# Kernel tuning notes

Measured on AMD Instinct MI355X. Metric: run time of the kernel, lower is better.

Reference implementation:

```python
import jax, jax.numpy as jnp
import numpy as np


def mha_col0(x0, w_in, b_in, w_out, b_out):
    # x0: [N, D]. torch MHA (1 head, batch_first=False): seq dim = N, this is the
    # batch-0 slice (the only one consumed by tmp[:, 0]).
    qkv = x0 @ w_in.T + b_in                     # [N, 3D]
    q, k, v = jnp.split(qkv, 3, axis=-1)         # each [N, D]
    scale = 1.0 / np.sqrt(np.float32(q.shape[-1]))
    attn = jax.nn.softmax((q * scale) @ k.T, axis=-1)   # [N, N]
    return (attn @ v) @ w_out.T + b_out          # [N, D]


def sage(x_src, x_dst, ei, w_l, b_l, w_r):
    # PyG SAGEConv with aggr='sum': out = lin_l(sum_j x_src[src_j]) + lin_r(x_dst)
    msg = x_src[ei[0]]                                            # [E, D] gather
    agg = jax.ops.segment_sum(msg, ei[1], num_segments=x_dst.shape[0])  # [Nd, D] scatter
    return agg @ w_l.T + b_l + x_dst @ w_r.T


def setup_inputs() -> dict:
    key = jax.random.key(0)
    ks = jax.random.split(key, 24)
    N, C, D, E = 8192, 6, 128, 262144
    s = 0.05
    p = lambda k, shape: jax.random.normal(k, shape, dtype=jnp.float32) * s
    return {
        "x_A": jax.random.normal(ks[0], (N, C, D), dtype=jnp.float32),
        "x_B": jax.random.normal(ks[1], (N, C, D), dtype=jnp.float32),
        "ei_AB": jax.random.randint(ks[2], (2, E), 0, N),
        "ei_BA": jax.random.randint(ks[3], (2, E), 0, N),
        "ei_AA": jax.random.randint(ks[4], (2, E), 0, N),
        "inW_A": p(ks[5], (3 * D, D)), "inB_A": p(ks[6], (3 * D,)),
        "outW_A": p(ks[7], (D, D)), "outB_A": p(ks[8], (D,)),
        "inW_B": p(ks[9], (3 * D, D)), "inB_B": p(ks[10], (3 * D,)),
        "outW_B": p(ks[11], (D, D)), "outB_B": p(ks[12], (D,)),
        "wl_AB": p(ks[13], (D, D)), "bl_AB": p(ks[14], (D,)), "wr_AB": p(ks[15], (D, D)),
        "wl_BA": p(ks[16], (D, D)), "bl_BA": p(ks[17], (D,)), "wr_BA": p(ks[18], (D, D)),
        "wl_AA": p(ks[19], (D, D)), "bl_AA": p(ks[20], (D,)), "wr_AA": p(ks[21], (D, D)),
    }


def reference(x_A, x_B, ei_AB, ei_BA, ei_AA,
              inW_A, inB_A, outW_A, outB_A,
              inW_B, inB_B, outW_B, outB_B,
              wl_AB, bl_AB, wr_AB,
              wl_BA, bl_BA, wr_BA,
              wl_AA, bl_AA, wr_AA):
    # per-type attention, keeping only column 0 (tmp[:, 0])
    h_A = mha_col0(x_A[:, 0], inW_A, inB_A, outW_A, outB_A)   # [N, D]
    h_B = mha_col0(x_B[:, 0], inW_B, inB_B, outW_B, outB_B)   # [N, D]
    # HeteroConv(aggr='sum'): B gets A->B; A gets B->A + A->A
    out_B = sage(h_A, h_B, ei_AB, wl_AB, bl_AB, wr_AB)
    out_A = (sage(h_B, h_A, ei_BA, wl_BA, bl_BA, wr_BA)
             + sage(h_A, h_A, ei_AA, wl_AA, bl_AA, wr_AA))
    # re-attach remaining column tokens (x is 3D)
    new_A = jnp.concatenate((out_A[:, None, :], x_A[:, 1:]), axis=1)  # [N, C, D]
    new_B = jnp.concatenate((out_B[:, None, :], x_B[:, 1:]), axis=1)
    return new_A, new_B
```

## Files before the change

### kernel.cpp

```cpp
#include <hip/hip_runtime.h>
#include <hip/hip_bf16.h>

typedef unsigned short u16;
typedef unsigned int u32;
typedef __attribute__((ext_vector_type(8))) short bf16x8;
typedef __attribute__((ext_vector_type(4))) short bf16x4;
typedef __attribute__((ext_vector_type(4))) float f32x4;
typedef __attribute__((ext_vector_type(16))) float f32x16;

#define MFMA(a,b,c)   __builtin_amdgcn_mfma_f32_16x16x32_bf16((a),(b),(c),0,0,0)
#define MFMA32(a,b,c) __builtin_amdgcn_mfma_f32_32x32x16_bf16((a),(b),(c),0,0,0)

__device__ __forceinline__ float bf2f(u16 u){
  union { float f; u32 i; } c; c.i = ((u32)u) << 16; return c.f;
}
__device__ __forceinline__ u16 f2bf(float f){
  __hip_bfloat16 h = __float2bfloat16(f);
  u16 u; __builtin_memcpy(&u, &h, 2); return u;
}
__device__ __forceinline__ bf16x8 ld8f(const float* p){
  bf16x8 r;
  #pragma unroll
  for (int i = 0; i < 8; i++) r[i] = (short)f2bf(p[i]);
  return r;
}
__device__ __forceinline__ u32 cvtpk(float a, float b){
  u32 r; asm volatile("v_cvt_pk_bf16_f32 %0, %1, %2" : "=v"(r) : "v"(a), "v"(b)); return r;
}
__device__ __forceinline__ void pl32swap(u32 &a, u32 &b){
  asm volatile("v_permlane32_swap_b32 %0, %1" : "+v"(a), "+v"(b));
}

struct WPrepArgs { const float* src[10]; int off[10]; int total4; };
__global__ __launch_bounds__(256) void prelude_kernel(
    WPrepArgs a, u16* __restrict__ wdst,
    const int* __restrict__ e0, const int* __restrict__ e1, const int* __restrict__ e2,
    int* __restrict__ cnt,
    const float* __restrict__ xA, float* __restrict__ outA,
    const float* __restrict__ xB, float* __restrict__ outB,
    int Nn, int E, int W, int HB, int TB)
{
  const int tid = threadIdx.x;
  int b = blockIdx.x;
  if (b < W) {
    int i = b * 256 + tid;
    if (i >= a.total4) return;
    int e = i * 4;
    int j = 0;
    #pragma unroll
    for (int k = 1; k < 10; k++) if (e >= a.off[k]) j = k;
    f32x4 v = *(const f32x4*)(a.src[j] + (e - a.off[j]));
    bf16x4 o;
    #pragma unroll
    for (int r = 0; r < 4; r++) o[r] = (short)f2bf(v[r]);
    *(bf16x4*)(wdst + e) = o;
    return;
  }
  b -= W;
  if (b < 3 * HB) {
    int t = b / HB;
    int e = (b % HB) * 256 + tid;
    if (e >= E) return;
    const int* ei = t == 0 ? e0 : (t == 1 ? e1 : e2);
    atomicAdd(&cnt[t * Nn + ei[E + e]], 1);
    return;
  }
  b -= 3 * HB;
  {
    int t = b / TB;
    int idx = (b % TB) * 256 + tid;
    if (idx >= Nn * 160) return;
    const float* x = t ? xB : xA;
    float* o = t ? outB : outA;
    int n = idx / 160, r = idx % 160;
    size_t off = (size_t)n * 768 + 128 + (size_t)r * 4;
    *(f32x4*)(o + off) = *(const f32x4*)(x + off);
  }
}

template<int XBF>
__global__ __launch_bounds__(256) void linear_kernel(
    const void* __restrict__ xA_, const u16* __restrict__ wA, const float* __restrict__ bA, u16* __restrict__ yA,
    const void* __restrict__ xB_, const u16* __restrict__ wB, const float* __restrict__ bB, u16* __restrict__ yB,
    u16* __restrict__ vtA_, u16* __restrict__ vtB_,
    int xstride, int ystride, int M, int N)
{
  const void* x_ = blockIdx.y ? xB_ : xA_;
  const u16* w = blockIdx.y ? wB : wA;
  const float* b = blockIdx.y ? bB : bA;
  u16* y = blockIdx.y ? yB : yA;
  u16* vt = blockIdx.y ? vtB_ : vtA_;
  const int lane = threadIdx.x & 63, wid = threadIdx.x >> 6;
  const int g = lane >> 4, l15 = lane & 15;
  const int row0 = blockIdx.x * 64 + wid * 16;

  bf16x8 a[4];
  if (XBF) {
    const u16* xr = (const u16*)x_ + (size_t)(row0 + l15) * xstride;
    #pragma unroll
    for (int kk = 0; kk < 4; kk++) a[kk] = *(const bf16x8*)(xr + kk * 32 + g * 8);
  } else {
    const float* xr = (const float*)x_ + (size_t)(row0 + l15) * xstride;
    #pragma unroll
    for (int kk = 0; kk < 4; kk++) a[kk] = ld8f(xr + kk * 32 + g * 8);
  }

  const f32x4 fz = {0.f, 0.f, 0.f, 0.f};
  for (int j0 = 0; j0 < M; j0 += 16) {
    f32x4 acc = fz;
    const u16* wr_ = w + (size_t)(j0 + l15) * 128;
    #pragma unroll
    for (int kk = 0; kk < 4; kk++)
      acc = MFMA(a[kk], *(const bf16x8*)(wr_ + kk * 32 + g * 8), acc);
    float bv = b[j0 + l15];
    if (j0 < 256 || vt == nullptr) {
      #pragma unroll
      for (int r = 0; r < 4; r++)
        y[(size_t)(row0 + g * 4 + r) * ystride + j0 + l15] = f2bf(acc[r] + bv);
    } else {
      bf16x4 o4;
      #pragma unroll
      for (int r = 0; r < 4; r++) o4[r] = (short)f2bf(acc[r] + bv);
      *(bf16x4*)(vt + (size_t)(j0 - 256 + l15) * N + row0 + g * 4) = o4;
    }
  }
}

__global__ __launch_bounds__(256, 2) void flash_kernel(
    const u16* __restrict__ qkvA, const u16* __restrict__ vtA,
    const u16* __restrict__ qkvB, const u16* __restrict__ vtB,
    u16* __restrict__ part_acc, float* __restrict__ part_ml,
    int N, int segsz, int SEG)
{
  __shared__ __align__(16) u16 Kt[2][64 * 128];
  __shared__ __align__(16) u16 Vtt[2][128 * 64];
  const int ty = blockIdx.z;
  const u16* qkv = ty ? qkvB : qkvA;
  const u16* vt  = ty ? vtB  : vtA;
  const int tid = threadIdx.x;
  const int lane = tid & 63, wid = tid >> 6;
  const int l31 = lane & 31, h = lane >> 5, l7 = lane & 7;
  const int q = blockIdx.x * 128 + wid * 32 + l31;
  const int seg = blockIdx.y;
  const int kvbase = seg * segsz;
  const float C = 0.088388347648318447f * 1.4426950408889634f;
  const float THR = 8.0f / C;

  int rk[4], ck[4], cks[4], rv[4], cv[4], cvs[4];
  #pragma unroll
  for (int i = 0; i < 4; i++) {
    int ch = tid + i * 256;
    rk[i] = ch >> 4; ck[i] = (ch & 15) * 8; cks[i] = ck[i] ^ ((rk[i] & 7) << 3);
    rv[i] = ch >> 3; cv[i] = (ch & 7) * 8;  cvs[i] = cv[i] ^ ((rv[i] & 7) << 3);
  }

  bf16x8 aQ[8];
  const u16* qr = qkv + (size_t)q * 256;
  #pragma unroll
  for (int kk = 0; kk < 8; kk++) aQ[kk] = *(const bf16x8*)(qr + kk * 16 + h * 8);

  f32x16 accO[4];
  #pragma unroll
  for (int d = 0; d < 4; d++) accO[d] = (f32x16)0.f;
  float m_ = -INFINITY, l_ = 0.f;

  {
    #pragma unroll
    for (int i = 0; i < 4; i++) {
      bf16x8 kv8 = *(const bf16x8*)(qkv + 128 + (size_t)(kvbase + rk[i]) * 256 + ck[i]);
      bf16x8 vv8 = *(const bf16x8*)(vt + (size_t)rv[i] * N + kvbase + cv[i]);
      *(bf16x8*)&Kt[0][rk[i] * 128 + cks[i]] = kv8;
      *(bf16x8*)&Vtt[0][rv[i] * 64 + cvs[i]] = vv8;
    }
  }
  __syncthreads();

  int cur = 0;
  for (int kt = 0; kt < segsz; kt += 64) {
    const bool pfch = (kt + 64 < segsz);
    bf16x8 kreg[4], vreg[4];
    if (pfch) {
      const int kv0n = kvbase + kt + 64;
      #pragma unroll
      for (int i = 0; i < 4; i++) {
        kreg[i] = *(const bf16x8*)(qkv + 128 + (size_t)(kv0n + rk[i]) * 256 + ck[i]);
        vreg[i] = *(const bf16x8*)(vt + (size_t)rv[i] * N + kv0n + cv[i]);
      }
    }

    const u16* KtC = Kt[cur];
    const u16* VtC = Vtt[cur];

    f32x16 sc0 = (f32x16)0.f, sc1 = (f32x16)0.f;
    __builtin_amdgcn_s_setprio(1);
    #pragma unroll
    for (int kk = 0; kk < 8; kk++) {
      const int co = ((kk * 2 + h) * 8) ^ (l7 << 3);
      bf16x8 aK0 = *(bf16x8*)&KtC[l31 * 128 + co];
      bf16x8 aK1 = *(bf16x8*)&KtC[(32 + l31) * 128 + co];
      sc0 = MFMA32(aK0, aQ[kk], sc0);
      sc1 = MFMA32(aK1, aQ[kk], sc1);
    }
    __builtin_amdgcn_s_setprio(0);

    float pmax = sc0[0];
    #pragma unroll
    for (int i = 1; i < 16; i++) pmax = fmaxf(pmax, sc0[i]);
    #pragma unroll
    for (int i = 0; i < 16; i++) pmax = fmaxf(pmax, sc1[i]);
    pmax = fmaxf(pmax, __shfl_xor(pmax, 32));
    if (!__all(pmax - m_ <= THR)) {
      float nm = fmaxf(m_, pmax);
      float corr = __builtin_exp2f((m_ - nm) * C);
      m_ = nm; l_ *= corr;
      #pragma unroll
      for (int d = 0; d < 4; d++)
        #pragma unroll
        for (int i = 0; i < 16; i++) accO[d][i] *= corr;
    }
    float sum = 0.f;
    #pragma unroll
    for (int i = 0; i < 16; i++) {
      float e0 = __builtin_exp2f((sc0[i] - m_) * C);
      float e1 = __builtin_exp2f((sc1[i] - m_) * C);
      sc0[i] = e0; sc1[i] = e1; sum += e0 + e1;
    }
    sum += __shfl_xor(sum, 32);
    l_ += sum;

    #pragma unroll
    for (int t = 0; t < 4; t++) {
      const int jA = (t & 1) * 2, jB = jA + 1;
      u32 a0, b0, a1, b1;
      if (t < 2) {
        a0 = cvtpk(sc0[jA * 4 + 0], sc0[jA * 4 + 1]);
        b0 = cvtpk(sc0[jB * 4 + 0], sc0[jB * 4 + 1]);
        a1 = cvtpk(sc0[jA * 4 + 2], sc0[jA * 4 + 3]);
        b1 = cvtpk(sc0[jB * 4 + 2], sc0[jB * 4 + 3]);
      } else {
        a0 = cvtpk(sc1[jA * 4 + 0], sc1[jA * 4 + 1]);
        b0 = cvtpk(sc1[jB * 4 + 0], sc1[jB * 4 + 1]);
        a1 = cvtpk(sc1[jA * 4 + 2], sc1[jA * 4 + 3]);
        b1 = cvtpk(sc1[jB * 4 + 2], sc1[jB * 4 + 3]);
      }
      pl32swap(a0, b0); pl32swap(a1, b1);
      union { u32 w[4]; bf16x8 v; } pf;
      pf.w[0] = a0; pf.w[1] = a1; pf.w[2] = b0; pf.w[3] = b1;
      __builtin_amdgcn_s_setprio(1);
      #pragma unroll
      for (int db = 0; db < 4; db++) {
        bf16x8 aV = *(bf16x8*)&VtC[(db * 32 + l31) * 64 + (((t * 2 + h) * 8) ^ (l7 << 3))];
        accO[db] = MFMA32(aV, pf.v, accO[db]);
      }
      __builtin_amdgcn_s_setprio(0);
    }

    if (pfch) {
      const int nb = cur ^ 1;
      #pragma unroll
      for (int i = 0; i < 4; i++) {
        *(bf16x8*)&Kt[nb][rk[i] * 128 + cks[i]] = kreg[i];
        *(bf16x8*)&Vtt[nb][rv[i] * 64 + cvs[i]] = vreg[i];
      }
    }
    __syncthreads();
    cur ^= 1;
  }

  const size_t pbase = ((size_t)(ty * SEG + seg) * N + q) * 128;
  #pragma unroll
  for (int d = 0; d < 4; d++)
    #pragma unroll
    for (int j = 0; j < 4; j++) {
      bf16x4 o4;
      #pragma unroll
      for (int r = 0; r < 4; r++) o4[r] = (short)f2bf(accO[d][j * 4 + r]);
      *(bf16x4*)(part_acc + pbase + d * 32 + j * 8 + h * 4) = o4;
    }
  if (h == 0) {
    float2 ml; ml.x = m_; ml.y = l_;
    *(float2*)(part_ml + ((size_t)(ty * SEG + seg) * N + q) * 2) = ml;
  }
}

__global__ __launch_bounds__(256) void combine_hproj_kernel(
    const u16* __restrict__ part_acc, const float* __restrict__ part_ml,
    const u16* __restrict__ woutA, const float* __restrict__ boutA, u16* __restrict__ hA,
    const u16* __restrict__ woutB, const float* __restrict__ boutB, u16* __restrict__ hB,
    int N, int SEG)
{
  __shared__ __align__(16) u16 ot[64 * 136];
  const int t = blockIdx.y;
  const u16* w = t ? woutB : woutA;
  const float* bb = t ? boutB : boutA;
  u16* hOut = t ? hB : hA;
  const int tid = threadIdx.x;
  const int row = tid >> 2, qt = tid & 3;
  const int grow = blockIdx.x * 64 + row;
  const float C = 0.088388347648318447f * 1.4426950408889634f;

  float m = -INFINITY;
  for (int s = 0; s < SEG; s++)
    m = fmaxf(m, part_ml[((size_t)(t * SEG + s) * N + grow) * 2]);
  float l = 0.f;
  float acc[32];
  #pragma unroll
  for (int i = 0; i < 32; i++) acc[i] = 0.f;
  for (int s = 0; s < SEG; s++) {
    const float* ml = part_ml + ((size_t)(t * SEG + s) * N + grow) * 2;
    float w8 = __builtin_exp2f((ml[0] - m) * C);
    l += w8 * ml[1];
    const u16* pa = part_acc + ((size_t)(t * SEG + s) * N + grow) * 128 + qt * 32;
    #pragma unroll
    for (int j = 0; j < 4; j++) {
      bf16x8 vch = *(const bf16x8*)(pa + j * 8);
      #pragma unroll
      for (int i = 0; i < 8; i++) acc[j * 8 + i] += w8 * bf2f((u16)vch[i]);
    }
  }
  const float inv = 1.f / l;
  #pragma unroll
  for (int j = 0; j < 4; j++) {
    bf16x8 oc;
    #pragma unroll
    for (int i = 0; i < 8; i++) oc[i] = (short)f2bf(acc[j * 8 + i] * inv);
    *(bf16x8*)&ot[row * 136 + qt * 32 + j * 8] = oc;
  }
  __syncthreads();

  const int lane = tid & 63, wid = tid >> 6;
  const int g = lane >> 4, l15 = lane & 15;
  const int row0 = wid * 16;
  bf16x8 a[4];
  #pragma unroll
  for (int kk = 0; kk < 4; kk++) a[kk] = *(bf16x8*)&ot[(row0 + l15) * 136 + kk * 32 + g * 8];
  const f32x4 fz = {0.f, 0.f, 0.f, 0.f};
  for (int j0 = 0; j0 < 128; j0 += 16) {
    f32x4 acc2 = fz;
    const u16* wr_ = w + (size_t)(j0 + l15) * 128;
    #pragma unroll
    for (int kk = 0; kk < 4; kk++)
      acc2 = MFMA(a[kk], *(const bf16x8*)(wr_ + kk * 32 + g * 8), acc2);
    float bv = bb[j0 + l15];
    #pragma unroll
    for (int r = 0; r < 4; r++)
      hOut[(size_t)(blockIdx.x * 64 + row0 + g * 4 + r) * 128 + j0 + l15] = f2bf(acc2[r] + bv);
  }
}

__global__ __launch_bounds__(1024) void scan_kernel(
    const int* __restrict__ cnt, int* __restrict__ off, int* __restrict__ work, int Nn)
{
  const int t = blockIdx.x;
  const int* c = cnt + t * Nn;
  int* o = off + t * (Nn + 1);
  int* w = work + t * Nn;
  __shared__ int part[1024];
  const int tid = threadIdx.x;
  const int base = tid * 8;
  int loc[8], s = 0;
  #pragma unroll
  for (int i = 0; i < 8; i++) { loc[i] = s; s += c[base + i]; }
  part[tid] = s;
  __syncthreads();
  #pragma unroll
  for (int st = 1; st < 1024; st <<= 1) {
    int v = (tid >= st) ? part[tid - st] : 0;
    __syncthreads();
    part[tid] += v;
    __syncthreads();
  }
  int pre = (tid == 0) ? 0 : part[tid - 1];
  #pragma unroll
  for (int i = 0; i < 8; i++) { int p = pre + loc[i]; o[base + i] = p; w[base + i] = p; }
  if (tid == 1023) o[Nn] = part[1023];
}

__global__ __launch_bounds__(256) void sortedges_kernel(
    const int* __restrict__ e0, const int* __restrict__ e1, const int* __restrict__ e2,
    int* __restrict__ work, int* __restrict__ ssrc, int Nn, int E)
{
  const int t = blockIdx.y;
  const int* ei = t == 0 ? e0 : (t == 1 ? e1 : e2);
  int e = blockIdx.x * 256 + threadIdx.x;
  if (e >= E) return;
  int s = ei[e], d = ei[E + e];
  int pos = atomicAdd(&work[t * Nn + d], 1);
  ssrc[(size_t)t * E + pos] = s;
}

__global__ __launch_bounds__(256) void aggregate_kernel(
    const u16* __restrict__ h0, const u16* __restrict__ h1, const u16* __restrict__ h2,
    const int* __restrict__ off, const int* __restrict__ ssrc,
    u16* __restrict__ agg, int Nn, int E)
{
  const int t = blockIdx.y;
  const u16* h = t == 0 ? h0 : (t == 1 ? h1 : h2);
  const int* o = off + t * (Nn + 1);
  const int* ss = ssrc + (size_t)t * E;
  u16* a = agg + (size_t)t * Nn * 128;
  const int wid = threadIdx.x >> 6, lane = threadIdx.x & 63;
  const int d = blockIdx.x * 4 + wid;
  const int s0 = o[d], s1 = o[d + 1];
  float a0 = 0.f, a1 = 0.f;
  int e = s0;
  for (; e + 3 < s1; e += 4) {
    int r0 = ss[e], r1 = ss[e + 1], r2 = ss[e + 2], r3 = ss[e + 3];
    u32 v0 = *(const u32*)(h + (size_t)r0 * 128 + lane * 2);
    u32 v1 = *(const u32*)(h + (size_t)r1 * 128 + lane * 2);
    u32 v2 = *(const u32*)(h + (size_t)r2 * 128 + lane * 2);
    u32 v3 = *(const u32*)(h + (size_t)r3 * 128 + lane * 2);
    a0 += bf2f((u16)(v0 & 0xffff)) + bf2f((u16)(v1 & 0xffff)) + bf2f((u16)(v2 & 0xffff)) + bf2f((u16)(v3 & 0xffff));
    a1 += bf2f((u16)(v0 >> 16)) + bf2f((u16)(v1 >> 16)) + bf2f((u16)(v2 >> 16)) + bf2f((u16)(v3 >> 16));
  }
  for (; e < s1; e++) {
    u32 v = *(const u32*)(h + (size_t)ss[e] * 128 + lane * 2);
    a0 += bf2f((u16)(v & 0xffff));
    a1 += bf2f((u16)(v >> 16));
  }
  *(u32*)(a + (size_t)d * 128 + lane * 2) = cvtpk(a0, a1);
}

__global__ __launch_bounds__(256) void sage_out_kernel(
    const u16* __restrict__ agg1, const u16* __restrict__ wl1, const float* __restrict__ bl1,
    const u16* __restrict__ h1, const u16* __restrict__ wr1,
    const u16* __restrict__ agg2, const u16* __restrict__ wl2, const float* __restrict__ bl2,
    const u16* __restrict__ h2, const u16* __restrict__ wr2,
    float* __restrict__ out)
{
  const int lane = threadIdx.x & 63, wid = threadIdx.x >> 6;
  const int g = lane >> 4, l15 = lane & 15;
  const int row0 = blockIdx.x * 64 + wid * 16;
  const bool two = (agg2 != nullptr);

  bf16x8 a1[4], aH1[4], a2[4], aH2[4];
  const u16* ar1 = agg1 + (size_t)(row0 + l15) * 128;
  const u16* hr1 = h1 + (size_t)(row0 + l15) * 128;
  #pragma unroll
  for (int kk = 0; kk < 4; kk++) {
    a1[kk] = *(const bf16x8*)(ar1 + kk * 32 + g * 8);
    aH1[kk] = *(const bf16x8*)(hr1 + kk * 32 + g * 8);
  }
  if (two) {
    const u16* ar2 = agg2 + (size_t)(row0 + l15) * 128;
    const u16* hr2 = h2 + (size_t)(row0 + l15) * 128;
    #pragma unroll
    for (int kk = 0; kk < 4; kk++) {
      a2[kk] = *(const bf16x8*)(ar2 + kk * 32 + g * 8);
      aH2[kk] = *(const bf16x8*)(hr2 + kk * 32 + g * 8);
    }
  }

  const f32x4 fz = {0.f, 0.f, 0.f, 0.f};
  for (int j0 = 0; j0 < 128; j0 += 16) {
    f32x4 acc = fz;
    const u16* w1 = wl1 + (size_t)(j0 + l15) * 128;
    const u16* w2 = wr1 + (size_t)(j0 + l15) * 128;
    #pragma unroll
    for (int kk = 0; kk < 4; kk++) {
      acc = MFMA(a1[kk], *(const bf16x8*)(w1 + kk * 32 + g * 8), acc);
      acc = MFMA(aH1[kk], *(const bf16x8*)(w2 + kk * 32 + g * 8), acc);
    }
    float bias = bl1[j0 + l15];
    if (two) {
      const u16* w3 = wl2 + (size_t)(j0 + l15) * 128;
      const u16* w4 = wr2 + (size_t)(j0 + l15) * 128;
      #pragma unroll
      for (int kk = 0; kk < 4; kk++) {
        acc = MFMA(a2[kk], *(const bf16x8*)(w3 + kk * 32 + g * 8), acc);
        acc = MFMA(aH2[kk], *(const bf16x8*)(w4 + kk * 32 + g * 8), acc);
      }
      bias += bl2[j0 + l15];
    }
    #pragma unroll
    for (int r = 0; r < 4; r++)
      out[(size_t)(row0 + g * 4 + r) * 768 + j0 + l15] = acc[r] + bias;
  }
}

extern "C" void kernel_launch(void* const* d_in, const int* in_sizes, int n_in,
                              void* d_out, int out_size, void* d_ws, size_t ws_size,
                              hipStream_t stream)
{
  const int D = 128, C = 6;
  const int N = in_sizes[0] / (C * D);
  const int E = in_sizes[2] / 2;

  const float* xA = (const float*)d_in[0];
  const float* xB = (const float*)d_in[1];
  const int* eiAB = (const int*)d_in[2];
  const int* eiBA = (const int*)d_in[3];
  const int* eiAA = (const int*)d_in[4];
  const float* inW_A  = (const float*)d_in[5];
  const float* inB_A  = (const float*)d_in[6];
  const float* outW_A = (const float*)d_in[7];
  const float* outB_A = (const float*)d_in[8];
  const float* inW_B  = (const float*)d_in[9];
  const float* inB_B  = (const float*)d_in[10];
  const float* outW_B = (const float*)d_in[11];
  const float* outB_B = (const float*)d_in[12];
  const float* wlAB = (const float*)d_in[13];
  const float* blAB = (const float*)d_in[14];
  const float* wrAB = (const float*)d_in[15];
  const float* wlBA = (const float*)d_in[16];
  const float* blBA = (const float*)d_in[17];
  const float* wrBA = (const float*)d_in[18];
  const float* wlAA = (const float*)d_in[19];
  const float* blAA = (const float*)d_in[20];
  const float* wrAA = (const float*)d_in[21];

  u16* qkvA = (u16*)d_ws;
  u16* qkvB = qkvA + (size_t)N * 256;
  u16* vtA  = qkvB + (size_t)N * 256;
  u16* vtB  = vtA + (size_t)D * N;
  u16* hA   = vtB + (size_t)D * N;
  u16* hB   = hA + (size_t)N * D;
  u16* wbf  = hB + (size_t)N * D;
  const int wsz[10] = {3*D*D, 3*D*D, D*D, D*D, D*D, D*D, D*D, D*D, D*D, D*D};
  const float* wsrc[10] = {inW_A, inW_B, outW_A, outW_B, wlAB, wrAB, wlBA, wrBA, wlAA, wrAA};
  WPrepArgs wp; int wtot = 0;
  for (int k = 0; k < 10; k++) { wp.src[k] = wsrc[k]; wp.off[k] = wtot; wtot += wsz[k]; }
  wp.total4 = wtot / 4;
  u16* w_inA  = wbf + wp.off[0];
  u16* w_inB  = wbf + wp.off[1];
  u16* w_outA = wbf + wp.off[2];
  u16* w_outB = wbf + wp.off[3];
  u16* w_wlAB = wbf + wp.off[4];
  u16* w_wrAB = wbf + wp.off[5];
  u16* w_wlBA = wbf + wp.off[6];
  u16* w_wrBA = wbf + wp.off[7];
  u16* w_wlAA = wbf + wp.off[8];
  u16* w_wrAA = wbf + wp.off[9];

  int* cnt  = (int*)(wbf + wtot);
  int* off  = cnt + 3 * N;
  int* work = off + 3 * (N + 1);
  int* ssrc = work + 3 * N;
  char* uni = (char*)(ssrc + 3 * E);
  size_t base_b = (size_t)(uni - (char*)d_ws);
  size_t agg_b = (size_t)3 * N * 128 * 2;
  auto part_b = [&](int S){ return (size_t)2 * S * N * 128 * 2 + (size_t)2 * S * N * 2 * 4; };
  int SEG = 4;
  while (SEG > 1 && ws_size < base_b + (part_b(SEG) > agg_b ? part_b(SEG) : agg_b)) SEG >>= 1;
  const int segsz = N / SEG;
  u16* part_acc = (u16*)uni;
  float* part_ml = (float*)(part_acc + (size_t)2 * SEG * N * 128);
  u16* aggAB = (u16*)uni;
  u16* aggBA = aggAB + (size_t)N * D;
  u16* aggAA = aggBA + (size_t)N * D;

  float* outA = (float*)d_out;
  float* outB = outA + (size_t)N * C * D;

  dim3 blk(256);
  const int W = (wp.total4 + 255) / 256;
  const int HB = (E + 255) / 256;
  const int TB = (N * 160 + 255) / 256;
  (void)hipMemsetAsync(cnt, 0, (size_t)3 * N * sizeof(int), stream);
  prelude_kernel<<<dim3(W + 3 * HB + 2 * TB), blk, 0, stream>>>(
      wp, wbf, eiAB, eiBA, eiAA, cnt, xA, outA, xB, outB, N, E, W, HB, TB);
  scan_kernel<<<dim3(3), dim3(1024), 0, stream>>>(cnt, off, work, N);
  sortedges_kernel<<<dim3(HB, 3), blk, 0, stream>>>(eiAB, eiBA, eiAA, work, ssrc, N, E);
  linear_kernel<0><<<dim3(N / 64, 2), blk, 0, stream>>>(xA, w_inA, inB_A, qkvA,
                                                        xB, w_inB, inB_B, qkvB,
                                                        vtA, vtB, C * D, 256, 384, N);
  flash_kernel<<<dim3(N / 128, SEG, 2), blk, 0, stream>>>(qkvA, vtA, qkvB, vtB,
                                                          part_acc, part_ml, N, segsz, SEG);
  combine_hproj_kernel<<<dim3(N / 64, 2), blk, 0, stream>>>(part_acc, part_ml,
                                                            w_outA, outB_A, hA,
                                                            w_outB, outB_B, hB, N, SEG);
  aggregate_kernel<<<dim3(N / 4, 3), blk, 0, stream>>>(hA, hB, hA, off, ssrc, aggAB, N, E);
  sage_out_kernel<<<dim3(N / 64), blk, 0, stream>>>(aggAB, w_wlAB, blAB, hB, w_wrAB,
                                                    nullptr, nullptr, nullptr, nullptr, nullptr, outB);
  sage_out_kernel<<<dim3(N / 64), blk, 0, stream>>>(aggBA, w_wlBA, blBA, hA, w_wrBA,
                                                    aggAA, w_wlAA, blAA, hA, w_wrAA, outA);
}
```

Baseline: 270.3 us.

## Fuse scan/sort into QKV and flash kernels, software-pipeline flash QK^T, prescale Q

Several changes land together. The edge-count scan now runs as extra blocks in the QKV projection kernel, and the edge sort runs as extra blocks in the flash attention kernel, which removes two launches. The two SAGE output launches become one 2-D launch. Q is prescaled by softmax_scale*log2(e) in the projection, so the flash and combine kernels drop the per-element multiply. The flash loop is restructured so the next tile's QK^T MFMAs are issued before the current tile's softmax and PV, using a triple-buffered V tile and ping-pong score registers. This adds register and LDS pressure. It also makes correctness rely on the scan finishing before the sort blocks run, which now holds only through stream ordering.

Measured after the change: 236.1 us. 12.6% less time.

```diff
diff --git a/kernel.cpp b/kernel.cpp
--- a/kernel.cpp
+++ b/kernel.cpp
@@ -30,6 +30,8 @@
 __device__ __forceinline__ void pl32swap(u32 &a, u32 &b){
   asm volatile("v_permlane32_swap_b32 %0, %1" : "+v"(a), "+v"(b));
 }
+
+#define QSCALE 0.12751741528681559f
 
 struct WPrepArgs { const float* src[10]; int off[10]; int total4; };
 __global__ __launch_bounds__(256) void prelude_kernel(
@@ -78,45 +80,71 @@
   }
 }
 
-template<int XBF>
-__global__ __launch_bounds__(256) void linear_kernel(
-    const void* __restrict__ xA_, const u16* __restrict__ wA, const float* __restrict__ bA, u16* __restrict__ yA,
-    const void* __restrict__ xB_, const u16* __restrict__ wB, const float* __restrict__ bB, u16* __restrict__ yB,
+__global__ __launch_bounds__(256) void qkv_scan_kernel(
+    const float* __restrict__ xA, const u16* __restrict__ wA, const float* __restrict__ bA, u16* __restrict__ yA,
+    const float* __restrict__ xB, const u16* __restrict__ wB, const float* __restrict__ bB, u16* __restrict__ yB,
     u16* __restrict__ vtA_, u16* __restrict__ vtB_,
-    int xstride, int ystride, int M, int N)
-{
-  const void* x_ = blockIdx.y ? xB_ : xA_;
-  const u16* w = blockIdx.y ? wB : wA;
-  const float* b = blockIdx.y ? bB : bA;
-  u16* y = blockIdx.y ? yB : yA;
-  u16* vt = blockIdx.y ? vtB_ : vtA_;
-  const int lane = threadIdx.x & 63, wid = threadIdx.x >> 6;
+    const int* __restrict__ cnt, int* __restrict__ off, int* __restrict__ work,
+    int Nn, int N, int LB)
+{
+  const int tid = threadIdx.x;
+  int b = blockIdx.x;
+  if (b >= 2 * LB) {
+    const int t = b - 2 * LB;
+    const int* c = cnt + t * Nn;
+    int* o = off + t * (Nn + 1);
+    int* w = work + t * Nn;
+    __shared__ int part[256];
+    const int base = tid * 32;
+    int loc[32], s = 0;
+    #pragma unroll
+    for (int i = 0; i < 32; i++) { loc[i] = s; s += c[base + i]; }
+    part[tid] = s;
+    __syncthreads();
+    #pragma unroll
+    for (int st = 1; st < 256; st <<= 1) {
+      int v = (tid >= st) ? part[tid - st] : 0;
+      __syncthreads();
+      part[tid] += v;
+      __syncthreads();
+    }
+    int pre = (tid == 0) ? 0 : part[tid - 1];
+    #pragma unroll
+    for (int i = 0; i < 32; i++) { int p = pre + loc[i]; o[base + i] = p; w[base + i] = p; }
+    if (tid == 255) o[Nn] = part[255];
+    return;
+  }
+  const int yb = b & 1, xb = b >> 1;
+  const float* x = yb ? xB : xA;
+  const u16* w = yb ? wB : wA;
+  const float* bb = yb ? bB : bA;
+  u16* y = yb ? yB : yA;
+  u16* vt = yb ? vtB_ : vtA_;
+  const int lane = tid & 63, wid = tid >> 6;
   const int g = lane >> 4, l15 = lane & 15;
-  const int row0 = blockIdx.x * 64 + wid * 16;
+  const int row0 = xb * 64 + wid * 16;
 
   bf16x8 a[4];
-  if (XBF) {
-    const u16* xr = (const u16*)x_ + (size_t)(row0 + l15) * xstride;
-    #pragma unroll
-    for (int kk = 0; kk < 4; kk++) a[kk] = *(const bf16x8*)(xr + kk * 32 + g * 8);
-  } else {
-    const float* xr = (const float*)x_ + (size_t)(row0 + l15) * xstride;
-    #pragma unroll
-    for (int kk = 0; kk < 4; kk++) a[kk] = ld8f(xr + kk * 32 + g * 8);
-  }
+  const float* xr = x + (size_t)(row0 + l15) * 768;
+  #pragma unroll
+  for (int kk = 0; kk < 4; kk++) a[kk] = ld8f(xr + kk * 32 + g * 8);
 
   const f32x4 fz = {0.f, 0.f, 0.f, 0.f};
-  for (int j0 = 0; j0 < M; j0 += 16) {
+  for (int j0 = 0; j0 < 384; j0 += 16) {
     f32x4 acc = fz;
     const u16* wr_ = w + (size_t)(j0 + l15) * 128;
     #pragma unroll
     for (int kk = 0; kk < 4; kk++)
       acc = MFMA(a[kk], *(const bf16x8*)(wr_ + kk * 32 + g * 8), acc);
-    float bv = b[j0 + l15];
-    if (j0 < 256 || vt == nullptr) {
+    float bv = bb[j0 + l15];
+    if (j0 < 128) {
       #pragma unroll
       for (int r = 0; r < 4; r++)
-        y[(size_t)(row0 + g * 4 + r) * ystride + j0 + l15] = f2bf(acc[r] + bv);
+        y[(size_t)(row0 + g * 4 + r) * 256 + j0 + l15] = f2bf((acc[r] + bv) * QSCALE);
+    } else if (j0 < 256) {
+      #pragma unroll
+      for (int r = 0; r < 4; r++)
+        y[(size_t)(row0 + g * 4 + r) * 256 + j0 + l15] = f2bf(acc[r] + bv);
     } else {
       bf16x4 o4;
       #pragma unroll
@@ -126,25 +154,40 @@
   }
 }
 
-__global__ __launch_bounds__(256, 2) void flash_kernel(
+__global__ __launch_bounds__(256, 2) void flash_sort_kernel(
     const u16* __restrict__ qkvA, const u16* __restrict__ vtA,
     const u16* __restrict__ qkvB, const u16* __restrict__ vtB,
     u16* __restrict__ part_acc, float* __restrict__ part_ml,
-    int N, int segsz, int SEG)
+    const int* __restrict__ e0, const int* __restrict__ e1, const int* __restrict__ e2,
+    int* __restrict__ work, int* __restrict__ ssrc,
+    int N, int segsz, int SEG, int NB128, int FB, int HB, int E)
 {
   __shared__ __align__(16) u16 Kt[2][64 * 128];
-  __shared__ __align__(16) u16 Vtt[2][128 * 64];
-  const int ty = blockIdx.z;
+  __shared__ __align__(16) u16 Vtt[3][128 * 64];
+  const int tid = threadIdx.x;
+  int b = blockIdx.x;
+  if (b >= FB) {
+    int sb = b - FB;
+    int t = sb / HB;
+    int e = (sb % HB) * 256 + tid;
+    if (e >= E) return;
+    const int* ei = t == 0 ? e0 : (t == 1 ? e1 : e2);
+    int s = ei[e], d = ei[E + e];
+    int pos = atomicAdd(&work[t * N + d], 1);
+    ssrc[(size_t)t * E + pos] = s;
+    return;
+  }
+  const int x = b % NB128;
+  const int rest = b / NB128;
+  const int seg = rest % SEG;
+  const int ty = rest / SEG;
   const u16* qkv = ty ? qkvB : qkvA;
   const u16* vt  = ty ? vtB  : vtA;
-  const int tid = threadIdx.x;
   const int lane = tid & 63, wid = tid >> 6;
   const int l31 = lane & 31, h = lane >> 5, l7 = lane & 7;
-  const int q = blockIdx.x * 128 + wid * 32 + l31;
-  const int seg = blockIdx.y;
+  const int q = x * 128 + wid * 32 + l31;
   const int kvbase = seg * segsz;
-  const float C = 0.088388347648318447f * 1.4426950408889634f;
-  const float THR = 8.0f / C;
+  const int nt = segsz >> 6;
 
   int rk[4], ck[4], cks[4], rv[4], cv[4], cvs[4];
   #pragma unroll
@@ -163,55 +206,79 @@
   #pragma unroll
   for (int d = 0; d < 4; d++) accO[d] = (f32x16)0.f;
   float m_ = -INFINITY, l_ = 0.f;
-
-  {
+  f32x16 scA[2], scB[2];
+  bf16x8 kreg[4], vreg[4];
+
+  #pragma unroll
+  for (int i = 0; i < 4; i++) {
+    kreg[i] = *(const bf16x8*)(qkv + 128 + (size_t)(kvbase + rk[i]) * 256 + ck[i]);
+    vreg[i] = *(const bf16x8*)(vt + (size_t)rv[i] * N + kvbase + cv[i]);
+  }
+  #pragma unroll
+  for (int i = 0; i < 4; i++) {
+    *(bf16x8*)&Kt[0][rk[i] * 128 + cks[i]] = kreg[i];
+    *(bf16x8*)&Vtt[0][rv[i] * 64 + cvs[i]] = vreg[i];
+  }
+  __syncthreads();
+  if (nt > 1) {
+    const int kv1 = kvbase + 64;
     #pragma unroll
     for (int i = 0; i < 4; i++) {
-      bf16x8 kv8 = *(const bf16x8*)(qkv + 128 + (size_t)(kvbase + rk[i]) * 256 + ck[i]);
-      bf16x8 vv8 = *(const bf16x8*)(vt + (size_t)rv[i] * N + kvbase + cv[i]);
-      *(bf16x8*)&Kt[0][rk[i] * 128 + cks[i]] = kv8;
-      *(bf16x8*)&Vtt[0][rv[i] * 64 + cvs[i]] = vv8;
-    }
-  }
-  __syncthreads();
-
-  int cur = 0;
-  for (int kt = 0; kt < segsz; kt += 64) {
-    const bool pfch = (kt + 64 < segsz);
-    bf16x8 kreg[4], vreg[4];
-    if (pfch) {
-      const int kv0n = kvbase + kt + 64;
+      kreg[i] = *(const bf16x8*)(qkv + 128 + (size_t)(kv1 + rk[i]) * 256 + ck[i]);
+      vreg[i] = *(const bf16x8*)(vt + (size_t)rv[i] * N + kv1 + cv[i]);
+    }
+  }
+  scA[0] = (f32x16)0.f; scA[1] = (f32x16)0.f;
+  #pragma unroll
+  for (int kk = 0; kk < 8; kk++) {
+    const int co = ((kk * 2 + h) * 8) ^ (l7 << 3);
+    bf16x8 aK0 = *(bf16x8*)&Kt[0][l31 * 128 + co];
+    bf16x8 aK1 = *(bf16x8*)&Kt[0][(32 + l31) * 128 + co];
+    scA[0] = MFMA32(aK0, aQ[kk], scA[0]);
+    scA[1] = MFMA32(aK1, aQ[kk], scA[1]);
+  }
+
+  int t = 0, vb = 0;
+  auto fstep = [&](f32x16* scIn, f32x16* scOut) {
+    const bool hasN = (t + 1 < nt);
+    const int kbN = (t + 1) & 1;
+    const int vbN = (vb + 1 == 3) ? 0 : vb + 1;
+    if (hasN) {
+      #pragma unroll
+      for (int i = 0; i < 4; i++) {
+        *(bf16x8*)&Kt[kbN][rk[i] * 128 + cks[i]] = kreg[i];
+        *(bf16x8*)&Vtt[vbN][rv[i] * 64 + cvs[i]] = vreg[i];
+      }
+    }
+    __syncthreads();
+    if (t + 2 < nt) {
+      const int kv0n = kvbase + (t + 2) * 64;
       #pragma unroll
       for (int i = 0; i < 4; i++) {
         kreg[i] = *(const bf16x8*)(qkv + 128 + (size_t)(kv0n + rk[i]) * 256 + ck[i]);
         vreg[i] = *(const bf16x8*)(vt + (size_t)rv[i] * N + kv0n + cv[i]);
       }
     }
-
-    const u16* KtC = Kt[cur];
-    const u16* VtC = Vtt[cur];
-
-    f32x16 sc0 = (f32x16)0.f, sc1 = (f32x16)0.f;
-    __builtin_amdgcn_s_setprio(1);
-    #pragma unroll
-    for (int kk = 0; kk < 8; kk++) {
-      const int co = ((kk * 2 + h) * 8) ^ (l7 << 3);
-      bf16x8 aK0 = *(bf16x8*)&KtC[l31 * 128 + co];
-      bf16x8 aK1 = *(bf16x8*)&KtC[(32 + l31) * 128 + co];
-      sc0 = MFMA32(aK0, aQ[kk], sc0);
-      sc1 = MFMA32(aK1, aQ[kk], sc1);
-    }
-    __builtin_amdgcn_s_setprio(0);
-
-    float pmax = sc0[0];
-    #pragma unroll
-    for (int i = 1; i < 16; i++) pmax = fmaxf(pmax, sc0[i]);
-    #pragma unroll
-    for (int i = 0; i < 16; i++) pmax = fmaxf(pmax, sc1[i]);
+    if (hasN) {
+      scOut[0] = (f32x16)0.f; scOut[1] = (f32x16)0.f;
+      #pragma unroll
+      for (int kk = 0; kk < 8; kk++) {
+        const int co = ((kk * 2 + h) * 8) ^ (l7 << 3);
+        bf16x8 aK0 = *(bf16x8*)&Kt[kbN][l31 * 128 + co];
+        bf16x8 aK1 = *(bf16x8*)&Kt[kbN][(32 + l31) * 128 + co];
+        scOut[0] = MFMA32(aK0, aQ[kk], scOut[0]);
+        scOut[1] = MFMA32(aK1, aQ[kk], scOut[1]);
+      }
+    }
+    float pmax = scIn[0][0];
+    #pragma unroll
+    for (int i = 1; i < 16; i++) pmax = fmaxf(pmax, scIn[0][i]);
+    #pragma unroll
+    for (int i = 0; i < 16; i++) pmax = fmaxf(pmax, scIn[1][i]);
     pmax = fmaxf(pmax, __shfl_xor(pmax, 32));
-    if (!__all(pmax - m_ <= THR)) {
+    if (!__all(pmax - m_ <= 8.0f)) {
       float nm = fmaxf(m_, pmax);
-      float corr = __builtin_exp2f((m_ - nm) * C);
+      float corr = __builtin_exp2f(m_ - nm);
       m_ = nm; l_ *= corr;
       #pragma unroll
       for (int d = 0; d < 4; d++)
@@ -221,51 +288,32 @@
     float sum = 0.f;
     #pragma unroll
     for (int i = 0; i < 16; i++) {
-      float e0 = __builtin_exp2f((sc0[i] - m_) * C);
-      float e1 = __builtin_exp2f((sc1[i] - m_) * C);
-      sc0[i] = e0; sc1[i] = e1; sum += e0 + e1;
+      float e0 = __builtin_exp2f(scIn[0][i] - m_);
+      float e1 = __builtin_exp2f(scIn[1][i] - m_);
+      scIn[0][i] = e0; scIn[1][i] = e1; sum += e0 + e1;
     }
     sum += __shfl_xor(sum, 32);
     l_ += sum;
-
-    #pragma unroll
-    for (int t = 0; t < 4; t++) {
-      const int jA = (t & 1) * 2, jB = jA + 1;
-      u32 a0, b0, a1, b1;
-      if (t < 2) {
-        a0 = cvtpk(sc0[jA * 4 + 0], sc0[jA * 4 + 1]);
-        b0 = cvtpk(sc0[jB * 4 + 0], sc0[jB * 4 + 1]);
-        a1 = cvtpk(sc0[jA * 4 + 2], sc0[jA * 4 + 3]);
-        b1 = cvtpk(sc0[jB * 4 + 2], sc0[jB * 4 + 3]);
-      } else {
-        a0 = cvtpk(sc1[jA * 4 + 0], sc1[jA * 4 + 1]);
-        b0 = cvtpk(sc1[jB * 4 + 0], sc1[jB * 4 + 1]);
-        a1 = cvtpk(sc1[jA * 4 + 2], sc1[jA * 4 + 3]);
-        b1 = cvtpk(sc1[jB * 4 + 2], sc1[jB * 4 + 3]);
-      }
+    #pragma unroll
+    for (int tt = 0; tt < 4; tt++) {
+      const f32x16& s_ = scIn[tt >> 1];
+      const int jA = (tt & 1) * 2, jB = jA + 1;
+      u32 a0 = cvtpk(s_[jA * 4 + 0], s_[jA * 4 + 1]);
+      u32 b0 = cvtpk(s_[jB * 4 + 0], s_[jB * 4 + 1]);
+      u32 a1 = cvtpk(s_[jA * 4 + 2], s_[jA * 4 + 3]);
+      u32 b1 = cvtpk(s_[jB * 4 + 2], s_[jB * 4 + 3]);
       pl32swap(a0, b0); pl32swap(a1, b1);
       union { u32 w[4]; bf16x8 v; } pf;
       pf.w[0] = a0; pf.w[1] = a1; pf.w[2] = b0; pf.w[3] = b1;
-      __builtin_amdgcn_s_setprio(1);
       #pragma unroll
       for (int db = 0; db < 4; db++) {
-        bf16x8 aV = *(bf16x8*)&VtC[(db * 32 + l31) * 64 + (((t * 2 + h) * 8) ^ (l7 << 3))];
+        bf16x8 aV = *(bf16x8*)&Vtt[vb][(db * 32 + l31) * 64 + (((tt * 2 + h) * 8) ^ (l7 << 3))];
         accO[db] = MFMA32(aV, pf.v, accO[db]);
       }
-      __builtin_amdgcn_s_setprio(0);
-    }
-
-    if (pfch) {
-      const int nb = cur ^ 1;
-      #pragma unroll
-      for (int i = 0; i < 4; i++) {
-        *(bf16x8*)&Kt[nb][rk[i] * 128 + cks[i]] = kreg[i];
-        *(bf16x8*)&Vtt[nb][rv[i] * 64 + cvs[i]] = vreg[i];
-      }
-    }
-    __syncthreads();
-    cur ^= 1;
-  }
+    }
+    vb = vbN; ++t;
+  };
+  while (t < nt) { fstep(scA, scB); fstep(scB, scA); }
 
   const size_t pbase = ((size_t)(ty * SEG + seg) * N + q) * 128;
   #pragma unroll
@@ -297,7 +345,6 @@
   const int tid = threadIdx.x;
   const int row = tid >> 2, qt = tid & 3;
   const int grow = blockIdx.x * 64 + row;
-  const float C = 0.088388347648318447f * 1.4426950408889634f;
 
   float m = -INFINITY;
   for (int s = 0; s < SEG; s++)
@@ -308,7 +355,7 @@
   for (int i = 0; i < 32; i++) acc[i] = 0.f;
   for (int s = 0; s < SEG; s++) {
     const float* ml = part_ml + ((size_t)(t * SEG + s) * N + grow) * 2;
-    float w8 = __builtin_exp2f((ml[0] - m) * C);
+    float w8 = __builtin_exp2f(ml[0] - m);
     l += w8 * ml[1];
     const u16* pa = part_acc + ((size_t)(t * SEG + s) * N + grow) * 128 + qt * 32;
     #pragma unroll
@@ -346,47 +393,6 @@
     for (int r = 0; r < 4; r++)
       hOut[(size_t)(blockIdx.x * 64 + row0 + g * 4 + r) * 128 + j0 + l15] = f2bf(acc2[r] + bv);
   }
-}
-
-__global__ __launch_bounds__(1024) void scan_kernel(
-    const int* __restrict__ cnt, int* __restrict__ off, int* __restrict__ work, int Nn)
-{
-  const int t = blockIdx.x;
-  const int* c = cnt + t * Nn;
-  int* o = off + t * (Nn + 1);
-  int* w = work + t * Nn;
-  __shared__ int part[1024];
-  const int tid = threadIdx.x;
-  const int base = tid * 8;
-  int loc[8], s = 0;
-  #pragma unroll
-  for (int i = 0; i < 8; i++) { loc[i] = s; s += c[base + i]; }
-  part[tid] = s;
-  __syncthreads();
-  #pragma unroll
-  for (int st = 1; st < 1024; st <<= 1) {
-    int v = (tid >= st) ? part[tid - st] : 0;
-    __syncthreads();
-    part[tid] += v;
-    __syncthreads();
-  }
-  int pre = (tid == 0) ? 0 : part[tid - 1];
-  #pragma unroll
-  for (int i = 0; i < 8; i++) { int p = pre + loc[i]; o[base + i] = p; w[base + i] = p; }
-  if (tid == 1023) o[Nn] = part[1023];
-}
-
-__global__ __launch_bounds__(256) void sortedges_kernel(
-    const int* __restrict__ e0, const int* __restrict__ e1, const int* __restrict__ e2,
-    int* __restrict__ work, int* __restrict__ ssrc, int Nn, int E)
-{
-  const int t = blockIdx.y;
-  const int* ei = t == 0 ? e0 : (t == 1 ? e1 : e2);
-  int e = blockIdx.x * 256 + threadIdx.x;
-  if (e >= E) return;
-  int s = ei[e], d = ei[E + e];
-  int pos = atomicAdd(&work[t * Nn + d], 1);
-  ssrc[(size_t)t * E + pos] = s;
 }
 
 __global__ __launch_bounds__(256) void aggregate_kernel(
@@ -422,18 +428,27 @@
 }
 
 __global__ __launch_bounds__(256) void sage_out_kernel(
-    const u16* __restrict__ agg1, const u16* __restrict__ wl1, const float* __restrict__ bl1,
-    const u16* __restrict__ h1, const u16* __restrict__ wr1,
-    const u16* __restrict__ agg2, const u16* __restrict__ wl2, const float* __restrict__ bl2,
-    const u16* __restrict__ h2, const u16* __restrict__ wr2,
-    float* __restrict__ out)
-{
+    const u16* __restrict__ aggAB, const u16* __restrict__ wlAB, const float* __restrict__ blAB,
+    const u16* __restrict__ hB, const u16* __restrict__ wrAB,
+    const u16* __restrict__ aggBA, const u16* __restrict__ wlBA, const float* __restrict__ blBA,
+    const u16* __restrict__ hA, const u16* __restrict__ wrBA,
+    const u16* __restrict__ aggAA, const u16* __restrict__ wlAA, const float* __restrict__ blAA,
+    const u16* __restrict__ wrAA,
+    float* __restrict__ outA, float* __restrict__ outB)
+{
+  const bool two = (blockIdx.y == 1);
+  const u16* agg1 = two ? aggBA : aggAB;
+  const u16* wl1  = two ? wlBA  : wlAB;
+  const float* bl1 = two ? blBA : blAB;
+  const u16* h1   = two ? hA : hB;
+  const u16* wr1  = two ? wrBA : wrAB;
+  float* out = two ? outA : outB;
+
   const int lane = threadIdx.x & 63, wid = threadIdx.x >> 6;
   const int g = lane >> 4, l15 = lane & 15;
   const int row0 = blockIdx.x * 64 + wid * 16;
-  const bool two = (agg2 != nullptr);
-
-  bf16x8 a1[4], aH1[4], a2[4], aH2[4];
+
+  bf16x8 a1[4], aH1[4], a2[4];
   const u16* ar1 = agg1 + (size_t)(row0 + l15) * 128;
   const u16* hr1 = h1 + (size_t)(row0 + l15) * 128;
   #pragma unroll
@@ -442,13 +457,10 @@
     aH1[kk] = *(const bf16x8*)(hr1 + kk * 32 + g * 8);
   }
   if (two) {
-    const u16* ar2 = agg2 + (size_t)(row0 + l15) * 128;
-    const u16* hr2 = h2 + (size_t)(row0 + l15) * 128;
-    #pragma unroll
-    for (int kk = 0; kk < 4; kk++) {
+    const u16* ar2 = aggAA + (size_t)(row0 + l15) * 128;
+    #pragma unroll
+    for (int kk = 0; kk < 4; kk++)
       a2[kk] = *(const bf16x8*)(ar2 + kk * 32 + g * 8);
-      aH2[kk] = *(const bf16x8*)(hr2 + kk * 32 + g * 8);
-    }
   }
 
   const f32x4 fz = {0.f, 0.f, 0.f, 0.f};
@@ -463,14 +475,14 @@
     }
     float bias = bl1[j0 + l15];
     if (two) {
-      const u16* w3 = wl2 + (size_t)(j0 + l15) * 128;
-      const u16* w4 = wr2 + (size_t)(j0 + l15) * 128;
+      const u16* w3 = wlAA + (size_t)(j0 + l15) * 128;
+      const u16* w4 = wrAA + (size_t)(j0 + l15) * 128;
       #pragma unroll
       for (int kk = 0; kk < 4; kk++) {
         acc = MFMA(a2[kk], *(const bf16x8*)(w3 + kk * 32 + g * 8), acc);
-        acc = MFMA(aH2[kk], *(const bf16x8*)(w4 + kk * 32 + g * 8), acc);
+        acc = MFMA(aH1[kk], *(const bf16x8*)(w4 + kk * 32 + g * 8), acc);
       }
-      bias += bl2[j0 + l15];
+      bias += blAA[j0 + l15];
     }
     #pragma unroll
     for (int r = 0; r < 4; r++)
@@ -556,22 +568,24 @@
   const int W = (wp.total4 + 255) / 256;
   const int HB = (E + 255) / 256;
   const int TB = (N * 160 + 255) / 256;
+  const int LB = N / 64;
+  const int NB128 = N / 128;
+  const int FB = NB128 * SEG * 2;
   (void)hipMemsetAsync(cnt, 0, (size_t)3 * N * sizeof(int), stream);
   prelude_kernel<<<dim3(W + 3 * HB + 2 * TB), blk, 0, stream>>>(
       wp, wbf, eiAB, eiBA, eiAA, cnt, xA, outA, xB, outB, N, E, W, HB, TB);
-  scan_kernel<<<dim3(3), dim3(1024), 0, stream>>>(cnt, off, work, N);
-  sortedges_kernel<<<dim3(HB, 3), blk, 0, stream>>>(eiAB, eiBA, eiAA, work, ssrc, N, E);
-  linear_kernel<0><<<dim3(N / 64, 2), blk, 0, stream>>>(xA, w_inA, inB_A, qkvA,
-                                                        xB, w_inB, inB_B, qkvB,
-                                                        vtA, vtB, C * D, 256, 384, N);
-  flash_kernel<<<dim3(N / 128, SEG, 2), blk, 0, stream>>>(qkvA, vtA, qkvB, vtB,
-                                                          part_acc, part_ml, N, segsz, SEG);
+  qkv_scan_kernel<<<dim3(2 * LB + 3), blk, 0, stream>>>(
+      xA, w_inA, inB_A, qkvA, xB, w_inB, inB_B, qkvB, vtA, vtB,
+      cnt, off, work, N, N, LB);
+  flash_sort_kernel<<<dim3(FB + 3 * HB), blk, 0, stream>>>(
+      qkvA, vtA, qkvB, vtB, part_acc, part_ml,
+      eiAB, eiBA, eiAA, work, ssrc, N, segsz, SEG, NB128, FB, HB, E);
   combine_hproj_kernel<<<dim3(N / 64, 2), blk, 0, stream>>>(part_acc, part_ml,
                                                             w_outA, outB_A, hA,
                                                             w_outB, outB_B, hB, N, SEG);
   aggregate_kernel<<<dim3(N / 4, 3), blk, 0, stream>>>(hA, hB, hA, off, ssrc, aggAB, N, E);
-  sage_out_kernel<<<dim3(N / 64), blk, 0, stream>>>(aggAB, w_wlAB, blAB, hB, w_wrAB,
-                                                    nullptr, nullptr, nullptr, nullptr, nullptr, outB);
-  sage_out_kernel<<<dim3(N / 64), blk, 0, stream>>>(aggBA, w_wlBA, blBA, hA, w_wrBA,
-                                                    aggAA, w_wlAA, blAA, hA, w_wrAA, outA);
-}
+  sage_out_kernel<<<dim3(N / 64, 2), blk, 0, stream>>>(
+      aggAB, w_wlAB, blAB, hB, w_wrAB,
+      aggBA, w_wlBA, blBA, hA, w_wrBA,
+      aggAA, w_wlAA, blAA, w_wrAA, outA, outB);
+}
```
